# Performance work log

Measured on AMD Instinct MI355X. Metric: run time of the kernel, lower is better.

Reference implementation:

```python
import jax, jax.numpy as jnp
import numpy as np

B = 32       # batch
IN_N = 32    # input capsules
IN_D = 16    # input capsule dim (== out_d)
H = 14       # input spatial
OUT_N = 32   # output capsules
OUT_D = 16
HO = 7       # parent grid h_out = w_out
HID = 64     # Linformer projection dim
EPS = 1e-5


def _gconv(x, w, groups):
    # x: [b, C, H, W], w: [C_out, C_in/groups, kh, kw]; stride 1, pad 1
    return jax.lax.conv_general_dilated(
        x, w, window_strides=(1, 1), padding=((1, 1), (1, 1)),
        dimension_numbers=("NCHW", "OIHW", "NCHW"), feature_group_count=groups)


def setup_inputs() -> dict:
    key = jax.random.key(0)
    ks = jax.random.split(key, 7)
    current_pose = jax.random.normal(ks[0], (B, IN_N, H, H, IN_D), dtype=jnp.float32)
    next_pose = jax.random.normal(ks[1], (B, OUT_N, HO, HO, OUT_D), dtype=jnp.float32)
    # grouped conv weights (torch layout OIHW, groups = IN_N)
    current_w = 0.05 * jax.random.normal(ks[2], (IN_N * IN_D, IN_D, 3, 3), dtype=jnp.float32)
    next_w = 0.05 * jax.random.normal(ks[3], (OUT_N * OUT_D, OUT_N * OUT_D // IN_N, 3, 3), dtype=jnp.float32)
    E_proj = 0.02 * jax.random.normal(ks[4], (IN_N, H * H, HID), dtype=jnp.float32)
    rel_embedd = jax.random.normal(ks[5], (IN_D, HO * HO), dtype=jnp.float32)
    ln_gamma = jnp.ones((OUT_D,), dtype=jnp.float32)
    ln_beta = jnp.zeros((OUT_D,), dtype=jnp.float32)
    return {
        "current_pose": current_pose, "next_pose": next_pose,
        "current_w": current_w, "next_w": next_w,
        "E_proj": E_proj, "rel_embedd": rel_embedd,
        "ln_gamma": ln_gamma, "ln_beta": ln_beta,
        "num_iter": 1,
    }


def reference(current_pose, next_pose, current_w, next_w, E_proj, rel_embedd,
              ln_gamma, ln_beta, num_iter):
    b = current_pose.shape[0]
    # 5D -> [b, n*d, H, W]
    cp = current_pose.transpose(0, 2, 3, 1, 4).reshape(b, H, H, IN_N * IN_D)
    cp = cp.transpose(0, 3, 1, 2)
    cp = _gconv(cp, current_w, IN_N)                       # [b, n*d, H, H]
    # headwise Linformer key projection
    cp = cp.reshape(b, IN_D, IN_N, 1, H * H)
    k = jnp.matmul(cp, E_proj)                             # [b, d, n, 1, HID]
    k = k.reshape(b, IN_D, IN_N * HID).transpose(0, 2, 1)  # [b, n*HID, d]
    rel = jnp.broadcast_to(rel_embedd.T[None], (b, HO * HO, IN_D))
    k = jnp.concatenate([k, rel], axis=1)                  # [b, N, d]

    # parent pose -> queries
    q = next_pose.transpose(0, 2, 3, 1, 4).reshape(b, HO, HO, OUT_N * OUT_D)
    q = q.transpose(0, 3, 1, 2)
    q = _gconv(q, next_w, IN_N)                            # [b, out_n*out_d, HO, HO]
    q = q.reshape(b, OUT_N * HO * HO, OUT_D)               # [b, J, d]

    dots = jnp.einsum("bje,bie->bji", q, k) * (IN_D ** -0.5)  # [b, J, N]
    dots = jax.nn.softmax(dots, axis=-2)                   # softmax over queries j
    out = jnp.einsum("bji,bie->bje", dots, k)              # [b, J, d]

    out = out.reshape(b, OUT_N * IN_D, HO, HO)
    out = _gconv(out, next_w, IN_N)
    out = out.reshape(b, OUT_N, HO, HO, IN_D)

    # LayerNorm over last dim (dropout rate = 0)
    mu = out.mean(-1, keepdims=True)
    var = ((out - mu) ** 2).mean(-1, keepdims=True)
    out = (out - mu) / jnp.sqrt(var + EPS) * ln_gamma + ln_beta
    return out
```

## Files before the change

### kernel.cpp

```cpp
#include <hip/hip_runtime.h>

typedef unsigned short u16;
typedef __attribute__((ext_vector_type(8))) short short8;
typedef __attribute__((ext_vector_type(4))) float floatx4;

#define MFMA16(a, b, c) __builtin_amdgcn_mfma_f32_16x16x32_bf16(a, b, c, 0, 0, 0)

__device__ inline u16 bf16rn(float x) {
    unsigned u = __float_as_uint(x);
    u += 0x7fffu + ((u >> 16) & 1u);
    return (u16)(u >> 16);
}
__device__ inline float bf16tof(u16 h) { return __uint_as_float(((unsigned)h) << 16); }
__device__ inline short8 ld8(const u16* p) { return *(const short8*)p; }

__global__ __launch_bounds__(256) void k_ecvt2(const float* __restrict__ E,
                                               const float* __restrict__ rel,
                                               const float* __restrict__ w,
                                               u16* __restrict__ EhT,
                                               u16* __restrict__ ElT,
                                               u16* __restrict__ Kh,
                                               u16* __restrict__ Kl,
                                               u16* __restrict__ KhT,
                                               u16* __restrict__ KlT,
                                               float* __restrict__ w2) {
    int blk = blockIdx.x, tid = threadIdx.x;
    if (blk < 32) {
        __shared__ float ep[196 * 65];
        int m = blk;
        const float* eb = E + (size_t)m * 12544;
        for (int t = tid; t < 12544; t += 256) {
            int p = t >> 6, h = t & 63;
            ep[p * 65 + h] = eb[t];
        }
        __syncthreads();
        for (int t = tid; t < 64 * 224; t += 256) {
            int h = t / 224, p = t % 224;
            float v = (p < 196) ? ep[p * 65 + h] : 0.f;
            u16 hi = bf16rn(v);
            u16 lo = bf16rn(v - bf16tof(hi));
            EhT[(size_t)m * 14336 + t] = hi;
            ElT[(size_t)m * 14336 + t] = lo;
        }
    } else if (blk < 64) {
        int b = blk - 32;
        size_t bK = (size_t)b * 2112;
        size_t bT = (size_t)b * 33792;
#pragma unroll
        for (int k = 0; k < 4; ++k) {
            int idx = tid + k * 256;
            int row = idx >> 4, e = idx & 15;
            int i = 2048 + row;
            float v = (row < 49) ? rel[e * 49 + row] : 0.f;
            u16 h = bf16rn(v);
            u16 l = bf16rn(v - bf16tof(h));
            Kh[(bK + i) * 16 + e] = h;
            Kl[(bK + i) * 16 + e] = l;
            KhT[bT + (size_t)e * 2112 + i] = h;
            KlT[bT + (size_t)e * 2112 + i] = l;
        }
    } else {
        int g0 = (blk - 64) * 4;
        for (int t = tid; t < 4 * 2304; t += 256) {
            int g = g0 + t / 2304, r = t % 2304;
            int oc = r / 144, rr = r % 144;
            w2[(size_t)g * 2304 + (rr / 9) * 144 + oc * 9 + (rr % 9)] =
                w[(size_t)g * 2304 + r];
        }
    }
}

__global__ __launch_bounds__(256) void k_conv14(const float* __restrict__ pose,
                                                const float* __restrict__ w2,
                                                float* __restrict__ out) {
    int blk = blockIdx.x;
    int oh = blk & 1, bg = blk >> 1;
    int tid = threadIdx.x;
    __shared__ float patch[16 * 256];
#pragma unroll
    for (int k = 0; k < 16; ++k) patch[k * 256 + tid] = 0.f;
    __syncthreads();
    const float* pin = pose + (size_t)bg * 3136;
    for (int t = tid; t < 3136; t += 256) {
        int p = t >> 4, ic = t & 15;
        int y = p / 14, x = p % 14;
        patch[ic * 256 + (y + 1) * 16 + (x + 1)] = pin[t];
    }
    __syncthreads();
    int g = bg & 31;
    const float* wg = w2 + (size_t)g * 2304 + oh * 72;
    float* po = out + (size_t)bg * 3136 + oh * 8 * 196;
    if (tid < 196) {
        int y = tid / 14, x = tid % 14;
        int base = (y + 1) * 16 + (x + 1);
        float acc[8];
#pragma unroll
        for (int oc = 0; oc < 8; ++oc) acc[oc] = 0.f;
        for (int ic = 0; ic < 16; ++ic) {
            const float* pr = patch + ic * 256 + base;
            float win[9];
#pragma unroll
            for (int ky = 0; ky < 3; ++ky)
#pragma unroll
                for (int kx = 0; kx < 3; ++kx)
                    win[ky * 3 + kx] = pr[(ky - 1) * 16 + (kx - 1)];
            const float* wi = wg + ic * 144;
#pragma unroll
            for (int oc = 0; oc < 8; ++oc)
#pragma unroll
                for (int kk = 0; kk < 9; ++kk)
                    acc[oc] += win[kk] * wi[oc * 9 + kk];
        }
#pragma unroll
        for (int oc = 0; oc < 8; ++oc) po[oc * 196 + tid] = acc[oc];
    }
}

__global__ __launch_bounds__(64) void k_conv7(const float* __restrict__ in,
                                              const float* __restrict__ in2,
                                              const float* __restrict__ w,
                                              float* __restrict__ out, int mode) {
    int blk = blockIdx.x;
    int oh = blk & 1, bg = blk >> 1;
    int tid = threadIdx.x;
    __shared__ float patch[16 * 144];
    for (int t = tid; t < 16 * 144; t += 64) patch[t] = 0.f;
    __syncthreads();
    const float* pin = in + (size_t)bg * 784;
    if (mode == 1) {
        for (int t = tid; t < 784; t += 64) {
            int p = t >> 4, ic = t & 15;
            int y = p / 7, x = p % 7;
            patch[ic * 144 + (y + 1) * 16 + (x + 1)] = pin[t];
        }
    } else {
        const float* pin2 = in2 + (size_t)bg * 784;
        for (int t = tid; t < 784; t += 64) {
            int ic = t / 49, p = t % 49;
            int y = p / 7, x = p % 7;
            patch[ic * 144 + (y + 1) * 16 + (x + 1)] = pin[t] + pin2[t];
        }
    }
    __syncthreads();
    int g = bg & 31;
    const float* wg = w + (size_t)g * 2304 + (size_t)oh * 8 * 144;
    float* po = out + (size_t)bg * 784 + (size_t)oh * 8 * 49;
    if (tid < 49) {
        int y = tid / 7, x = tid % 7;
        int base = (y + 1) * 16 + (x + 1);
        float acc[8];
#pragma unroll
        for (int oc = 0; oc < 8; ++oc) acc[oc] = 0.f;
        for (int ic = 0; ic < 16; ++ic) {
            const float* pr = patch + ic * 144 + base;
            float win[9];
#pragma unroll
            for (int ky = 0; ky < 3; ++ky)
#pragma unroll
                for (int kx = 0; kx < 3; ++kx)
                    win[ky * 3 + kx] = pr[(ky - 1) * 16 + (kx - 1)];
            const float* wi = wg + ic * 9;
#pragma unroll
            for (int oc = 0; oc < 8; ++oc)
#pragma unroll
                for (int kk = 0; kk < 9; ++kk)
                    acc[oc] += win[kk] * wi[oc * 144 + kk];
        }
#pragma unroll
        for (int oc = 0; oc < 8; ++oc) po[oc * 49 + tid] = acc[oc];
    }
}

__global__ __launch_bounds__(256) void k_kproj2(const float* __restrict__ cpconv,
                                                const u16* __restrict__ EhT,
                                                const u16* __restrict__ ElT,
                                                u16* __restrict__ Kh,
                                                u16* __restrict__ Kl,
                                                u16* __restrict__ KhT,
                                                u16* __restrict__ KlT) {
    int blk = blockIdx.x;
    int b = blk >> 5, m = blk & 31;
    int wave = threadIdx.x >> 6, lane = threadIdx.x & 63;
    int ht = wave;
    int n = lane & 15, quad = lane >> 4;

    const float* arow = cpconv + ((size_t)b * 512 + (size_t)n * 32 + m) * 196;
    const u16* bhrow = EhT + ((size_t)m * 64 + ht * 16 + n) * 224;
    const u16* blrow = ElT + ((size_t)m * 64 + ht * 16 + n) * 224;

    floatx4 c = {0.f, 0.f, 0.f, 0.f};
#pragma unroll
    for (int pc = 0; pc < 7; ++pc) {
        int p0 = pc * 32 + quad * 8;
        float av[8];
        if (p0 <= 188) {
            float4 x = *(const float4*)(arow + p0);
            float4 y = *(const float4*)(arow + p0 + 4);
            av[0]=x.x; av[1]=x.y; av[2]=x.z; av[3]=x.w;
            av[4]=y.x; av[5]=y.y; av[6]=y.z; av[7]=y.w;
        } else {
#pragma unroll
            for (int k2 = 0; k2 < 8; ++k2) av[k2] = (p0 + k2 < 196) ? arow[p0 + k2] : 0.f;
        }
        short8 ah, al;
#pragma unroll
        for (int k2 = 0; k2 < 8; ++k2) {
            u16 h = bf16rn(av[k2]);
            ah[k2] = (short)h;
            al[k2] = (short)bf16rn(av[k2] - bf16tof(h));
        }
        short8 bh = ld8(bhrow + pc * 32 + quad * 8);
        short8 bl = ld8(blrow + pc * 32 + quad * 8);
        c = MFMA16(ah, bh, c);
        c = MFMA16(ah, bl, c);
        c = MFMA16(al, bh, c);
    }
    int i = m * 64 + ht * 16 + n;
    size_t bK = (size_t)b * 2112;
    size_t bT = (size_t)b * 33792;
    u16 h[4], l[4];
#pragma unroll
    for (int r = 0; r < 4; ++r) {
        h[r] = bf16rn(c[r]);
        l[r] = bf16rn(c[r] - bf16tof(h[r]));
    }
    *(uint2*)(Kh + (bK + i) * 16 + quad * 4) =
        make_uint2((unsigned)h[0] | ((unsigned)h[1] << 16), (unsigned)h[2] | ((unsigned)h[3] << 16));
    *(uint2*)(Kl + (bK + i) * 16 + quad * 4) =
        make_uint2((unsigned)l[0] | ((unsigned)l[1] << 16), (unsigned)l[2] | ((unsigned)l[3] << 16));
#pragma unroll
    for (int r = 0; r < 4; ++r) {
        KhT[bT + (size_t)(quad * 4 + r) * 2112 + i] = h[r];
        KlT[bT + (size_t)(quad * 4 + r) * 2112 + i] = l[r];
    }
}

__global__ __launch_bounds__(256) void k_cvt(const float* __restrict__ qconv,
                                             u16* __restrict__ Qp) {
    int gid = blockIdx.x * 256 + threadIdx.x;
    const float4* q4 = (const float4*)(qconv + (size_t)gid * 16);
    float4 t0 = q4[0], t1 = q4[1], t2 = q4[2], t3 = q4[3];
    float v[16] = {t0.x,t0.y,t0.z,t0.w, t1.x,t1.y,t1.z,t1.w,
                   t2.x,t2.y,t2.z,t2.w, t3.x,t3.y,t3.z,t3.w};
    unsigned hw[8], lw[8];
#pragma unroll
    for (int t = 0; t < 8; ++t) {
        float x0 = v[2*t] * 0.25f, x1 = v[2*t+1] * 0.25f;
        u16 h0 = bf16rn(x0), h1 = bf16rn(x1);
        u16 l0 = bf16rn(x0 - bf16tof(h0)), l1 = bf16rn(x1 - bf16tof(h1));
        hw[t] = (unsigned)h0 | ((unsigned)h1 << 16);
        lw[t] = (unsigned)l0 | ((unsigned)l1 << 16);
    }
    uint4* r4 = (uint4*)(Qp + (size_t)gid * 32);
    r4[0] = make_uint4(hw[0], hw[1], hw[2], hw[3]);
    r4[1] = make_uint4(hw[4], hw[5], hw[6], hw[7]);
    r4[2] = make_uint4(lw[0], lw[1], lw[2], lw[3]);
    r4[3] = make_uint4(lw[4], lw[5], lw[6], lw[7]);
}

__global__ __launch_bounds__(256) void k_stats4(const u16* __restrict__ Qp,
                                                const u16* __restrict__ Kh,
                                                const u16* __restrict__ Kl,
                                                float* __restrict__ dpart) {
    int blk = blockIdx.x;
    int b = blk / 34; int rem = blk % 34; int jh = rem / 17; int tb = rem % 17;
    int wave = threadIdx.x >> 6, lane = threadIdx.x & 63;
    int it2 = tb * 4 + wave;
    if (it2 >= 66) return;
    int ibase = it2 * 32;
    int n = lane & 15, quad = lane >> 4;
    size_t bK = (size_t)b * 2112;
    const u16* kb = Kh + (bK + ibase + n) * 16 + (quad & 1) * 8;
    const u16* lb = Kl + (bK + ibase + n) * 16 + (quad & 1) * 8;
    short8 bh0 = ld8(kb), bh1 = ld8(kb + 256);
    short8 bl0 = ld8(lb), bl1 = ld8(lb + 256);
    const u16* qb = Qp + (size_t)b * 50176 + (size_t)jh * 49 * 512 + n * 32 + quad * 8;
    floatx4 d0 = {0.f,0.f,0.f,0.f}, d1 = {0.f,0.f,0.f,0.f};
    short8 a0 = ld8(qb), a1 = ld8(qb + 512);
    for (int c = 0; c < 49; ++c) {
        short8 a2 = (c + 2 < 49) ? ld8(qb + (size_t)(c + 2) * 512) : a0;
        floatx4 s0 = {0.f,0.f,0.f,0.f}, s1 = {0.f,0.f,0.f,0.f};
        s0 = MFMA16(a0, bh0, s0);
        s0 = MFMA16(a0, bl0, s0);
        s1 = MFMA16(a0, bh1, s1);
        s1 = MFMA16(a0, bl1, s1);
        d0.x += __expf(s0.x); d0.y += __expf(s0.y);
        d0.z += __expf(s0.z); d0.w += __expf(s0.w);
        d1.x += __expf(s1.x); d1.y += __expf(s1.y);
        d1.z += __expf(s1.z); d1.w += __expf(s1.w);
        a0 = a1; a1 = a2;
    }
    float t0 = d0.x + d0.y + d0.z + d0.w;
    float t1 = d1.x + d1.y + d1.z + d1.w;
    t0 += __shfl_xor(t0, 16); t0 += __shfl_xor(t0, 32);
    t1 += __shfl_xor(t1, 16); t1 += __shfl_xor(t1, 32);
    if (quad == 0) {
        dpart[(size_t)jh * 67584 + bK + ibase + n]      = t0;
        dpart[(size_t)jh * 67584 + bK + ibase + 16 + n] = t1;
    }
}

__global__ __launch_bounds__(256) void k_pv5(const u16* __restrict__ Qp,
                                             const u16* __restrict__ Kh,
                                             const u16* __restrict__ Kl,
                                             const u16* __restrict__ KhT,
                                             const u16* __restrict__ KlT,
                                             const float* __restrict__ dpart,
                                             float* __restrict__ opart) {
    __shared__ __align__(16) u16 sH[2][32][16];
    __shared__ __align__(16) u16 sL[2][32][16];
    __shared__ __align__(16) u16 tH[2][16][32];
    __shared__ __align__(16) u16 tL[2][16][32];
    __shared__ __align__(16) u16 w16[4][16][40];
    __shared__ float rll[2][32];

    int blk = blockIdx.x;
    int b = blk / 50; int rem = blk % 50; int jtb = rem >> 1; int ih = rem & 1;
    int tid = threadIdx.x, wave = tid >> 6, lane = tid & 63;
    int n = lane & 15, quad = lane >> 4, qh = quad & 1;
    int jt = jtb * 4 + wave;
    int jtc = jt < 98 ? jt : 97;
    int i0 = ih * 1056;
    size_t bK = (size_t)b * 2112;
    size_t bT = (size_t)b * 33792;
    const float* d0p = dpart + bK;
    const float* d1p = dpart + 67584 + bK;

    short8 aq = ld8(Qp + ((size_t)b * 1568 + (size_t)jtc * 16 + n) * 32 + quad * 8);

    int role = wave, L = lane;
    uint4 sreg; float dv = 1.f;
    auto ldchunk = [&](int c) {
        int i0c = i0 + c * 32;
        if (role == 0)      sreg = *(const uint4*)(Kh  + (bK + i0c + (L >> 1)) * 16 + (L & 1) * 8);
        else if (role == 1) sreg = *(const uint4*)(Kl  + (bK + i0c + (L >> 1)) * 16 + (L & 1) * 8);
        else if (role == 2) sreg = *(const uint4*)(KhT + bT + (size_t)(L >> 2) * 2112 + i0c + (L & 3) * 8);
        else {
            sreg = *(const uint4*)(KlT + bT + (size_t)(L >> 2) * 2112 + i0c + (L & 3) * 8);
            if (L < 32) dv = d0p[i0c + L] + d1p[i0c + L];
        }
    };
    auto stchunk = [&](int bf) {
        if (role == 0)      *(uint4*)(&sH[bf][L >> 1][(L & 1) * 8]) = sreg;
        else if (role == 1) *(uint4*)(&sL[bf][L >> 1][(L & 1) * 8]) = sreg;
        else if (role == 2) *(uint4*)(&tH[bf][L >> 2][(L & 3) * 8]) = sreg;
        else {
            *(uint4*)(&tL[bf][L >> 2][(L & 3) * 8]) = sreg;
            if (L < 32) rll[bf][L] = 1.0f / dv;
        }
    };

    floatx4 o = {0.f, 0.f, 0.f, 0.f};

    ldchunk(0); stchunk(0); ldchunk(1);
    __syncthreads();
    for (int c = 0; c < 33; ++c) {
        int cb = c & 1;
        short8 sh0 = ld8(&sH[cb][n][qh * 8]);
        short8 sh1 = ld8(&sH[cb][16 + n][qh * 8]);
        short8 sl0 = ld8(&sL[cb][n][qh * 8]);
        short8 sl1 = ld8(&sL[cb][16 + n][qh * 8]);
        short8 th  = ld8(&tH[cb][n][quad * 8]);
        short8 tl  = ld8(&tL[cb][n][quad * 8]);
        float r0 = rll[cb][n], r1 = rll[cb][16 + n];
        floatx4 s0 = {0.f,0.f,0.f,0.f};
        s0 = MFMA16(aq, sh0, s0);
        s0 = MFMA16(aq, sl0, s0);
        floatx4 s1 = {0.f,0.f,0.f,0.f};
        s1 = MFMA16(aq, sh1, s1);
        s1 = MFMA16(aq, sl1, s1);
#pragma unroll
        for (int r = 0; r < 4; ++r) {
            float w0 = __expf(s0[r]) * r0;
            float w1 = __expf(s1[r]) * r1;
            w16[wave][quad * 4 + r][n]      = (u16)(__float_as_uint(w0) >> 16);
            w16[wave][quad * 4 + r][16 + n] = (u16)(__float_as_uint(w1) >> 16);
        }
        asm volatile("s_waitcnt lgkmcnt(0)" ::: "memory");
        short8 aw = ld8(&w16[wave][n][quad * 8]);
        o = MFMA16(aw, th, o);
        o = MFMA16(aw, tl, o);
        if (c < 32) stchunk((c + 1) & 1);
        if (c < 31) ldchunk(c + 2);
        __syncthreads();
    }
    if (jt < 98) {
        float* ob = opart + (size_t)ih * 802816 + ((size_t)b * 1568 + (size_t)jt * 16) * 16;
#pragma unroll
        for (int r = 0; r < 4; ++r) ob[(quad * 4 + r) * 16 + n] = o[r];
    }
}

__global__ __launch_bounds__(256) void k_ln(const float* __restrict__ x,
                                            const float* __restrict__ gamma,
                                            const float* __restrict__ beta,
                                            float* __restrict__ out, int ngroups) {
    int g = blockIdx.x * 256 + threadIdx.x;
    if (g >= ngroups) return;
    const float4* xp = (const float4*)(x + (size_t)g * 16);
    float4 x0 = xp[0], x1 = xp[1], x2 = xp[2], x3 = xp[3];
    float sum = x0.x + x0.y + x0.z + x0.w + x1.x + x1.y + x1.z + x1.w
              + x2.x + x2.y + x2.z + x2.w + x3.x + x3.y + x3.z + x3.w;
    float mu = sum * 0.0625f;
    float var = 0.f;
    var += (x0.x-mu)*(x0.x-mu) + (x0.y-mu)*(x0.y-mu) + (x0.z-mu)*(x0.z-mu) + (x0.w-mu)*(x0.w-mu);
    var += (x1.x-mu)*(x1.x-mu) + (x1.y-mu)*(x1.y-mu) + (x1.z-mu)*(x1.z-mu) + (x1.w-mu)*(x1.w-mu);
    var += (x2.x-mu)*(x2.x-mu) + (x2.y-mu)*(x2.y-mu) + (x2.z-mu)*(x2.z-mu) + (x2.w-mu)*(x2.w-mu);
    var += (x3.x-mu)*(x3.x-mu) + (x3.y-mu)*(x3.y-mu) + (x3.z-mu)*(x3.z-mu) + (x3.w-mu)*(x3.w-mu);
    float rstd = rsqrtf(var * 0.0625f + 1e-5f);
    const float4* gp = (const float4*)gamma;
    const float4* bp = (const float4*)beta;
    float4 g0 = gp[0], g1 = gp[1], g2 = gp[2], g3 = gp[3];
    float4 be0 = bp[0], be1 = bp[1], be2 = bp[2], be3 = bp[3];
    float4 o0, o1, o2, o3;
    o0.x = (x0.x-mu)*rstd*g0.x + be0.x; o0.y = (x0.y-mu)*rstd*g0.y + be0.y;
    o0.z = (x0.z-mu)*rstd*g0.z + be0.z; o0.w = (x0.w-mu)*rstd*g0.w + be0.w;
    o1.x = (x1.x-mu)*rstd*g1.x + be1.x; o1.y = (x1.y-mu)*rstd*g1.y + be1.y;
    o1.z = (x1.z-mu)*rstd*g1.z + be1.z; o1.w = (x1.w-mu)*rstd*g1.w + be1.w;
    o2.x = (x2.x-mu)*rstd*g2.x + be2.x; o2.y = (x2.y-mu)*rstd*g2.y + be2.y;
    o2.z = (x2.z-mu)*rstd*g2.z + be2.z; o2.w = (x2.w-mu)*rstd*g2.w + be2.w;
    o3.x = (x3.x-mu)*rstd*g3.x + be3.x; o3.y = (x3.y-mu)*rstd*g3.y + be3.y;
    o3.z = (x3.z-mu)*rstd*g3.z + be3.z; o3.w = (x3.w-mu)*rstd*g3.w + be3.w;
    float4* op = (float4*)(out + (size_t)g * 16);
    op[0] = o0; op[1] = o1; op[2] = o2; op[3] = o3;
}

extern "C" void kernel_launch(void* const* d_in, const int* in_sizes, int n_in,
                              void* d_out, int out_size, void* d_ws, size_t ws_size,
                              hipStream_t stream) {
    const float* current_pose = (const float*)d_in[0];
    const float* next_pose    = (const float*)d_in[1];
    const float* current_w    = (const float*)d_in[2];
    const float* next_w       = (const float*)d_in[3];
    const float* E_proj       = (const float*)d_in[4];
    const float* rel          = (const float*)d_in[5];
    const float* ln_gamma     = (const float*)d_in[6];
    const float* ln_beta      = (const float*)d_in[7];
    float* out = (float*)d_out;
    float* ws  = (float*)d_ws;

    float* cpconv = ws;
    float* conv2  = ws;
    float* opart  = ws + 802816;
    float* dpart  = ws + 2408448;
    float* qconv  = ws + 3211264;
    float* w2     = ws + 4014080;
    u16*   ub     = (u16*)(ws + 4087808);
    u16* Qp  = ub;
    u16* Kh  = ub + 1605632;
    u16* Kl  = ub + 2686976;
    u16* KhT = ub + 3768320;
    u16* KlT = ub + 4849664;
    u16* EhT = ub + 5931008;
    u16* ElT = ub + 6389760;

    k_ecvt2 <<<72,   256, 0, stream>>>(E_proj, rel, current_w, EhT, ElT,
                                       Kh, Kl, KhT, KlT, w2);
    k_conv14<<<2048, 256, 0, stream>>>(current_pose, w2, cpconv);
    k_conv7 <<<2048, 64,  0, stream>>>(next_pose, next_pose, next_w, qconv, 1);
    k_cvt   <<<196,  256, 0, stream>>>(qconv, Qp);
    k_kproj2<<<1024, 256, 0, stream>>>(cpconv, EhT, ElT, Kh, Kl, KhT, KlT);
    k_stats4<<<1088, 256, 0, stream>>>(Qp, Kh, Kl, dpart);
    k_pv5   <<<1600, 256, 0, stream>>>(Qp, Kh, Kl, KhT, KlT, dpart, opart);
    k_conv7 <<<2048, 64,  0, stream>>>(opart, opart + 802816, next_w, conv2, 0);
    k_ln    <<<196,  256, 0, stream>>>(conv2, ln_gamma, ln_beta, out, 50176);
}
```

Baseline: 232.3 us.

## Fuse q-conv with bf16 split, conv with layernorm, prescale K, pipeline PV loop

The query conv now writes split-bf16 Q directly, which removes the separate conversion kernel and its fp32 round trip. The output conv is fused with LayerNorm and sums three partial buffers. A new k_kscale kernel folds the per-key softmax denominators into the transposed K once, so the PV loop no longer divides by them. The PV kernel splits the key range three ways instead of two and software-pipelines the second MFMA pair one chunk behind. The cost is an extra kernel launch plus a K rewrite pass, more blocks, and K rounding applied twice.

```diff
diff --git a/kernel.cpp b/kernel.cpp
--- a/kernel.cpp
+++ b/kernel.cpp
@@ -116,37 +116,27 @@
     }
 }
 
-__global__ __launch_bounds__(64) void k_conv7(const float* __restrict__ in,
-                                              const float* __restrict__ in2,
-                                              const float* __restrict__ w,
-                                              float* __restrict__ out, int mode) {
-    int blk = blockIdx.x;
-    int oh = blk & 1, bg = blk >> 1;
+__global__ __launch_bounds__(128) void k_conv7q(const float* __restrict__ pose,
+                                                const float* __restrict__ w,
+                                                u16* __restrict__ Qp) {
+    int bg = blockIdx.x;
     int tid = threadIdx.x;
     __shared__ float patch[16 * 144];
-    for (int t = tid; t < 16 * 144; t += 64) patch[t] = 0.f;
-    __syncthreads();
-    const float* pin = in + (size_t)bg * 784;
-    if (mode == 1) {
-        for (int t = tid; t < 784; t += 64) {
-            int p = t >> 4, ic = t & 15;
-            int y = p / 7, x = p % 7;
-            patch[ic * 144 + (y + 1) * 16 + (x + 1)] = pin[t];
-        }
-    } else {
-        const float* pin2 = in2 + (size_t)bg * 784;
-        for (int t = tid; t < 784; t += 64) {
-            int ic = t / 49, p = t % 49;
-            int y = p / 7, x = p % 7;
-            patch[ic * 144 + (y + 1) * 16 + (x + 1)] = pin[t] + pin2[t];
-        }
+    __shared__ float cvout[784];
+    for (int t = tid; t < 16 * 144; t += 128) patch[t] = 0.f;
+    __syncthreads();
+    const float* pin = pose + (size_t)bg * 784;
+    for (int t = tid; t < 784; t += 128) {
+        int p = t >> 4, ic = t & 15;
+        int y = p / 7, x = p % 7;
+        patch[ic * 144 + (y + 1) * 16 + (x + 1)] = pin[t];
     }
     __syncthreads();
     int g = bg & 31;
+    int oh = tid >> 6, lt = tid & 63;
     const float* wg = w + (size_t)g * 2304 + (size_t)oh * 8 * 144;
-    float* po = out + (size_t)bg * 784 + (size_t)oh * 8 * 49;
-    if (tid < 49) {
-        int y = tid / 7, x = tid % 7;
+    if (lt < 49) {
+        int y = lt / 7, x = lt % 7;
         int base = (y + 1) * 16 + (x + 1);
         float acc[8];
 #pragma unroll
@@ -167,7 +157,28 @@
                     acc[oc] += win[kk] * wi[oc * 144 + kk];
         }
 #pragma unroll
-        for (int oc = 0; oc < 8; ++oc) po[oc * 49 + tid] = acc[oc];
+        for (int oc = 0; oc < 8; ++oc) cvout[(oh * 8 + oc) * 49 + lt] = acc[oc];
+    }
+    __syncthreads();
+    if (tid < 49) {
+        float v[16];
+#pragma unroll
+        for (int k = 0; k < 16; ++k) v[k] = cvout[tid * 16 + k];
+        unsigned hw[8], lw[8];
+#pragma unroll
+        for (int t = 0; t < 8; ++t) {
+            float x0 = v[2*t] * 0.25f, x1 = v[2*t+1] * 0.25f;
+            u16 h0 = bf16rn(x0), h1 = bf16rn(x1);
+            u16 l0 = bf16rn(x0 - bf16tof(h0)), l1 = bf16rn(x1 - bf16tof(h1));
+            hw[t] = (unsigned)h0 | ((unsigned)h1 << 16);
+            lw[t] = (unsigned)l0 | ((unsigned)l1 << 16);
+        }
+        size_t j = (size_t)bg * 49 + tid;
+        uint4* r4 = (uint4*)(Qp + j * 32);
+        r4[0] = make_uint4(hw[0], hw[1], hw[2], hw[3]);
+        r4[1] = make_uint4(hw[4], hw[5], hw[6], hw[7]);
+        r4[2] = make_uint4(lw[0], lw[1], lw[2], lw[3]);
+        r4[3] = make_uint4(lw[4], lw[5], lw[6], lw[7]);
     }
 }
 
@@ -233,29 +244,6 @@
         KhT[bT + (size_t)(quad * 4 + r) * 2112 + i] = h[r];
         KlT[bT + (size_t)(quad * 4 + r) * 2112 + i] = l[r];
     }
-}
-
-__global__ __launch_bounds__(256) void k_cvt(const float* __restrict__ qconv,
-                                             u16* __restrict__ Qp) {
-    int gid = blockIdx.x * 256 + threadIdx.x;
-    const float4* q4 = (const float4*)(qconv + (size_t)gid * 16);
-    float4 t0 = q4[0], t1 = q4[1], t2 = q4[2], t3 = q4[3];
-    float v[16] = {t0.x,t0.y,t0.z,t0.w, t1.x,t1.y,t1.z,t1.w,
-                   t2.x,t2.y,t2.z,t2.w, t3.x,t3.y,t3.z,t3.w};
-    unsigned hw[8], lw[8];
-#pragma unroll
-    for (int t = 0; t < 8; ++t) {
-        float x0 = v[2*t] * 0.25f, x1 = v[2*t+1] * 0.25f;
-        u16 h0 = bf16rn(x0), h1 = bf16rn(x1);
-        u16 l0 = bf16rn(x0 - bf16tof(h0)), l1 = bf16rn(x1 - bf16tof(h1));
-        hw[t] = (unsigned)h0 | ((unsigned)h1 << 16);
-        lw[t] = (unsigned)l0 | ((unsigned)l1 << 16);
-    }
-    uint4* r4 = (uint4*)(Qp + (size_t)gid * 32);
-    r4[0] = make_uint4(hw[0], hw[1], hw[2], hw[3]);
-    r4[1] = make_uint4(hw[4], hw[5], hw[6], hw[7]);
-    r4[2] = make_uint4(lw[0], lw[1], lw[2], lw[3]);
-    r4[3] = make_uint4(lw[4], lw[5], lw[6], lw[7]);
 }
 
 __global__ __launch_bounds__(256) void k_stats4(const u16* __restrict__ Qp,
@@ -300,89 +288,125 @@
     }
 }
 
-__global__ __launch_bounds__(256) void k_pv5(const u16* __restrict__ Qp,
+__global__ __launch_bounds__(256) void k_kscale(const float* __restrict__ dpart,
+                                                u16* __restrict__ KhT,
+                                                u16* __restrict__ KlT) {
+    int blk = blockIdx.x;
+    int b = blk >> 2, q = blk & 3;
+    int tid = threadIdx.x;
+    size_t bT = (size_t)b * 33792;
+    const float* d0 = dpart + (size_t)b * 2112;
+    const float* d1 = dpart + 67584 + (size_t)b * 2112;
+    for (int t = tid; t < 1056; t += 256) {
+        int v = q * 1056 + t;
+        int e = v / 264, i8 = (v % 264) * 8;
+        size_t off = bT + (size_t)e * 2112 + i8;
+        uint4 hv = *(uint4*)(KhT + off);
+        uint4 lv = *(uint4*)(KlT + off);
+        float4 da = *(const float4*)(d0 + i8), db = *(const float4*)(d0 + i8 + 4);
+        float4 ea = *(const float4*)(d1 + i8), eb = *(const float4*)(d1 + i8 + 4);
+        float rl[8] = {1.f/(da.x+ea.x), 1.f/(da.y+ea.y), 1.f/(da.z+ea.z), 1.f/(da.w+ea.w),
+                       1.f/(db.x+eb.x), 1.f/(db.y+eb.y), 1.f/(db.z+eb.z), 1.f/(db.w+eb.w)};
+        unsigned hu[4] = {hv.x, hv.y, hv.z, hv.w};
+        unsigned lu[4] = {lv.x, lv.y, lv.z, lv.w};
+        unsigned ho[4], lo4[4];
+#pragma unroll
+        for (int k = 0; k < 4; ++k) {
+            u16 h0 = (u16)hu[k], h1 = (u16)(hu[k] >> 16);
+            u16 l0 = (u16)lu[k], l1 = (u16)(lu[k] >> 16);
+            float v0 = (bf16tof(h0) + bf16tof(l0)) * rl[2*k];
+            float v1 = (bf16tof(h1) + bf16tof(l1)) * rl[2*k+1];
+            u16 nh0 = bf16rn(v0), nh1 = bf16rn(v1);
+            u16 nl0 = bf16rn(v0 - bf16tof(nh0)), nl1 = bf16rn(v1 - bf16tof(nh1));
+            ho[k]  = (unsigned)nh0 | ((unsigned)nh1 << 16);
+            lo4[k] = (unsigned)nl0 | ((unsigned)nl1 << 16);
+        }
+        *(uint4*)(KhT + off) = make_uint4(ho[0], ho[1], ho[2], ho[3]);
+        *(uint4*)(KlT + off) = make_uint4(lo4[0], lo4[1], lo4[2], lo4[3]);
+    }
+}
+
+__global__ __launch_bounds__(256) void k_pv6(const u16* __restrict__ Qp,
                                              const u16* __restrict__ Kh,
                                              const u16* __restrict__ Kl,
                                              const u16* __restrict__ KhT,
                                              const u16* __restrict__ KlT,
-                                             const float* __restrict__ dpart,
                                              float* __restrict__ opart) {
     __shared__ __align__(16) u16 sH[2][32][16];
     __shared__ __align__(16) u16 sL[2][32][16];
     __shared__ __align__(16) u16 tH[2][16][32];
     __shared__ __align__(16) u16 tL[2][16][32];
-    __shared__ __align__(16) u16 w16[4][16][40];
-    __shared__ float rll[2][32];
+    __shared__ __align__(16) u16 w16[4][2][16][40];
 
     int blk = blockIdx.x;
-    int b = blk / 50; int rem = blk % 50; int jtb = rem >> 1; int ih = rem & 1;
+    int b = blk / 75; int rem = blk % 75; int jtb = rem / 3; int ih = rem % 3;
     int tid = threadIdx.x, wave = tid >> 6, lane = tid & 63;
     int n = lane & 15, quad = lane >> 4, qh = quad & 1;
     int jt = jtb * 4 + wave;
     int jtc = jt < 98 ? jt : 97;
-    int i0 = ih * 1056;
+    int i0 = ih * 704;
     size_t bK = (size_t)b * 2112;
     size_t bT = (size_t)b * 33792;
-    const float* d0p = dpart + bK;
-    const float* d1p = dpart + 67584 + bK;
 
     short8 aq = ld8(Qp + ((size_t)b * 1568 + (size_t)jtc * 16 + n) * 32 + quad * 8);
 
     int role = wave, L = lane;
-    uint4 sreg; float dv = 1.f;
+    uint4 sreg;
     auto ldchunk = [&](int c) {
         int i0c = i0 + c * 32;
         if (role == 0)      sreg = *(const uint4*)(Kh  + (bK + i0c + (L >> 1)) * 16 + (L & 1) * 8);
         else if (role == 1) sreg = *(const uint4*)(Kl  + (bK + i0c + (L >> 1)) * 16 + (L & 1) * 8);
         else if (role == 2) sreg = *(const uint4*)(KhT + bT + (size_t)(L >> 2) * 2112 + i0c + (L & 3) * 8);
-        else {
-            sreg = *(const uint4*)(KlT + bT + (size_t)(L >> 2) * 2112 + i0c + (L & 3) * 8);
-            if (L < 32) dv = d0p[i0c + L] + d1p[i0c + L];
-        }
+        else                sreg = *(const uint4*)(KlT + bT + (size_t)(L >> 2) * 2112 + i0c + (L & 3) * 8);
     };
     auto stchunk = [&](int bf) {
         if (role == 0)      *(uint4*)(&sH[bf][L >> 1][(L & 1) * 8]) = sreg;
         else if (role == 1) *(uint4*)(&sL[bf][L >> 1][(L & 1) * 8]) = sreg;
         else if (role == 2) *(uint4*)(&tH[bf][L >> 2][(L & 3) * 8]) = sreg;
-        else {
-            *(uint4*)(&tL[bf][L >> 2][(L & 3) * 8]) = sreg;
-            if (L < 32) rll[bf][L] = 1.0f / dv;
-        }
+        else                *(uint4*)(&tL[bf][L >> 2][(L & 3) * 8]) = sreg;
     };
 
     floatx4 o = {0.f, 0.f, 0.f, 0.f};
+    short8 thp = {}, tlp = {};
 
     ldchunk(0); stchunk(0); ldchunk(1);
     __syncthreads();
-    for (int c = 0; c < 33; ++c) {
+    for (int c = 0; c < 22; ++c) {
         int cb = c & 1;
+        short8 th  = ld8(&tH[cb][n][quad * 8]);
+        short8 tl  = ld8(&tL[cb][n][quad * 8]);
         short8 sh0 = ld8(&sH[cb][n][qh * 8]);
         short8 sh1 = ld8(&sH[cb][16 + n][qh * 8]);
         short8 sl0 = ld8(&sL[cb][n][qh * 8]);
         short8 sl1 = ld8(&sL[cb][16 + n][qh * 8]);
-        short8 th  = ld8(&tH[cb][n][quad * 8]);
-        short8 tl  = ld8(&tL[cb][n][quad * 8]);
-        float r0 = rll[cb][n], r1 = rll[cb][16 + n];
+        short8 aw = {};
+        if (c > 0) aw = ld8(&w16[wave][1 - cb][n][quad * 8]);
         floatx4 s0 = {0.f,0.f,0.f,0.f};
         s0 = MFMA16(aq, sh0, s0);
         s0 = MFMA16(aq, sl0, s0);
         floatx4 s1 = {0.f,0.f,0.f,0.f};
         s1 = MFMA16(aq, sh1, s1);
         s1 = MFMA16(aq, sl1, s1);
+        if (c > 0) {
+            o = MFMA16(aw, thp, o);
+            o = MFMA16(aw, tlp, o);
+        }
 #pragma unroll
         for (int r = 0; r < 4; ++r) {
-            float w0 = __expf(s0[r]) * r0;
-            float w1 = __expf(s1[r]) * r1;
-            w16[wave][quad * 4 + r][n]      = (u16)(__float_as_uint(w0) >> 16);
-            w16[wave][quad * 4 + r][16 + n] = (u16)(__float_as_uint(w1) >> 16);
-        }
-        asm volatile("s_waitcnt lgkmcnt(0)" ::: "memory");
-        short8 aw = ld8(&w16[wave][n][quad * 8]);
-        o = MFMA16(aw, th, o);
-        o = MFMA16(aw, tl, o);
-        if (c < 32) stchunk((c + 1) & 1);
-        if (c < 31) ldchunk(c + 2);
+            float w0 = __expf(s0[r]);
+            float w1 = __expf(s1[r]);
+            w16[wave][cb][quad * 4 + r][n]      = (u16)(__float_as_uint(w0) >> 16);
+            w16[wave][cb][quad * 4 + r][16 + n] = (u16)(__float_as_uint(w1) >> 16);
+        }
+        thp = th; tlp = tl;
+        if (c + 1 < 22) stchunk((c + 1) & 1);
+        if (c + 2 < 22) ldchunk(c + 2);
         __syncthreads();
+    }
+    {
+        short8 aw = ld8(&w16[wave][1][n][quad * 8]);
+        o = MFMA16(aw, thp, o);
+        o = MFMA16(aw, tlp, o);
     }
     if (jt < 98) {
         float* ob = opart + (size_t)ih * 802816 + ((size_t)b * 1568 + (size_t)jt * 16) * 16;
@@ -391,38 +415,73 @@
     }
 }
 
-__global__ __launch_bounds__(256) void k_ln(const float* __restrict__ x,
-                                            const float* __restrict__ gamma,
-                                            const float* __restrict__ beta,
-                                            float* __restrict__ out, int ngroups) {
-    int g = blockIdx.x * 256 + threadIdx.x;
-    if (g >= ngroups) return;
-    const float4* xp = (const float4*)(x + (size_t)g * 16);
-    float4 x0 = xp[0], x1 = xp[1], x2 = xp[2], x3 = xp[3];
-    float sum = x0.x + x0.y + x0.z + x0.w + x1.x + x1.y + x1.z + x1.w
-              + x2.x + x2.y + x2.z + x2.w + x3.x + x3.y + x3.z + x3.w;
-    float mu = sum * 0.0625f;
-    float var = 0.f;
-    var += (x0.x-mu)*(x0.x-mu) + (x0.y-mu)*(x0.y-mu) + (x0.z-mu)*(x0.z-mu) + (x0.w-mu)*(x0.w-mu);
-    var += (x1.x-mu)*(x1.x-mu) + (x1.y-mu)*(x1.y-mu) + (x1.z-mu)*(x1.z-mu) + (x1.w-mu)*(x1.w-mu);
-    var += (x2.x-mu)*(x2.x-mu) + (x2.y-mu)*(x2.y-mu) + (x2.z-mu)*(x2.z-mu) + (x2.w-mu)*(x2.w-mu);
-    var += (x3.x-mu)*(x3.x-mu) + (x3.y-mu)*(x3.y-mu) + (x3.z-mu)*(x3.z-mu) + (x3.w-mu)*(x3.w-mu);
-    float rstd = rsqrtf(var * 0.0625f + 1e-5f);
-    const float4* gp = (const float4*)gamma;
-    const float4* bp = (const float4*)beta;
-    float4 g0 = gp[0], g1 = gp[1], g2 = gp[2], g3 = gp[3];
-    float4 be0 = bp[0], be1 = bp[1], be2 = bp[2], be3 = bp[3];
-    float4 o0, o1, o2, o3;
-    o0.x = (x0.x-mu)*rstd*g0.x + be0.x; o0.y = (x0.y-mu)*rstd*g0.y + be0.y;
-    o0.z = (x0.z-mu)*rstd*g0.z + be0.z; o0.w = (x0.w-mu)*rstd*g0.w + be0.w;
-    o1.x = (x1.x-mu)*rstd*g1.x + be1.x; o1.y = (x1.y-mu)*rstd*g1.y + be1.y;
-    o1.z = (x1.z-mu)*rstd*g1.z + be1.z; o1.w = (x1.w-mu)*rstd*g1.w + be1.w;
-    o2.x = (x2.x-mu)*rstd*g2.x + be2.x; o2.y = (x2.y-mu)*rstd*g2.y + be2.y;
-    o2.z = (x2.z-mu)*rstd*g2.z + be2.z; o2.w = (x2.w-mu)*rstd*g2.w + be2.w;
-    o3.x = (x3.x-mu)*rstd*g3.x + be3.x; o3.y = (x3.y-mu)*rstd*g3.y + be3.y;
-    o3.z = (x3.z-mu)*rstd*g3.z + be3.z; o3.w = (x3.w-mu)*rstd*g3.w + be3.w;
-    float4* op = (float4*)(out + (size_t)g * 16);
-    op[0] = o0; op[1] = o1; op[2] = o2; op[3] = o3;
+__global__ __launch_bounds__(128) void k_conv7ln(const float* __restrict__ op0,
+                                                 const float* __restrict__ op1,
+                                                 const float* __restrict__ op2,
+                                                 const float* __restrict__ w,
+                                                 const float* __restrict__ gamma,
+                                                 const float* __restrict__ beta,
+                                                 float* __restrict__ out) {
+    int bg = blockIdx.x;
+    int tid = threadIdx.x;
+    __shared__ float patch[16 * 144];
+    __shared__ float cvout[784];
+    for (int t = tid; t < 16 * 144; t += 128) patch[t] = 0.f;
+    __syncthreads();
+    const float* p0 = op0 + (size_t)bg * 784;
+    const float* p1 = op1 + (size_t)bg * 784;
+    const float* p2 = op2 + (size_t)bg * 784;
+    for (int t = tid; t < 784; t += 128) {
+        int ic = t / 49, p = t % 49;
+        int y = p / 7, x = p % 7;
+        patch[ic * 144 + (y + 1) * 16 + (x + 1)] = p0[t] + p1[t] + p2[t];
+    }
+    __syncthreads();
+    int g = bg & 31;
+    int oh = tid >> 6, lt = tid & 63;
+    const float* wg = w + (size_t)g * 2304 + (size_t)oh * 8 * 144;
+    if (lt < 49) {
+        int y = lt / 7, x = lt % 7;
+        int base = (y + 1) * 16 + (x + 1);
+        float acc[8];
+#pragma unroll
+        for (int oc = 0; oc < 8; ++oc) acc[oc] = 0.f;
+        for (int ic = 0; ic < 16; ++ic) {
+            const float* pr = patch + ic * 144 + base;
+            float win[9];
+#pragma unroll
+            for (int ky = 0; ky < 3; ++ky)
+#pragma unroll
+                for (int kx = 0; kx < 3; ++kx)
+                    win[ky * 3 + kx] = pr[(ky - 1) * 16 + (kx - 1)];
+            const float* wi = wg + ic * 9;
+#pragma unroll
+            for (int oc = 0; oc < 8; ++oc)
+#pragma unroll
+                for (int kk = 0; kk < 9; ++kk)
+                    acc[oc] += win[kk] * wi[oc * 144 + kk];
+        }
+#pragma unroll
+        for (int oc = 0; oc < 8; ++oc) cvout[(oh * 8 + oc) * 49 + lt] = acc[oc];
+    }
+    __syncthreads();
+    if (tid < 49) {
+        float v[16];
+        float sum = 0.f;
+#pragma unroll
+        for (int k = 0; k < 16; ++k) { v[k] = cvout[tid * 16 + k]; sum += v[k]; }
+        float mu = sum * 0.0625f;
+        float var = 0.f;
+#pragma unroll
+        for (int k = 0; k < 16; ++k) { float d = v[k] - mu; var += d * d; }
+        float rstd = rsqrtf(var * 0.0625f + 1e-5f);
+        float4 o4[4];
+#pragma unroll
+        for (int k = 0; k < 16; ++k)
+            ((float*)o4)[k] = (v[k] - mu) * rstd * gamma[k] + beta[k];
+        float4* po = (float4*)(out + (size_t)bg * 784 + (size_t)tid * 16);
+        po[0] = o4[0]; po[1] = o4[1]; po[2] = o4[2]; po[3] = o4[3];
+    }
 }
 
 extern "C" void kernel_launch(void* const* d_in, const int* in_sizes, int n_in,
@@ -440,12 +499,10 @@
     float* ws  = (float*)d_ws;
 
     float* cpconv = ws;
-    float* conv2  = ws;
-    float* opart  = ws + 802816;
+    float* opart  = ws;
     float* dpart  = ws + 2408448;
-    float* qconv  = ws + 3211264;
-    float* w2     = ws + 4014080;
-    u16*   ub     = (u16*)(ws + 4087808);
+    float* w2     = ws + 3211264;
+    u16*   ub     = (u16*)(ws + 3284992);
     u16* Qp  = ub;
     u16* Kh  = ub + 1605632;
     u16* Kl  = ub + 2686976;
@@ -454,14 +511,15 @@
     u16* EhT = ub + 5931008;
     u16* ElT = ub + 6389760;
 
-    k_ecvt2 <<<72,   256, 0, stream>>>(E_proj, rel, current_w, EhT, ElT,
-                                       Kh, Kl, KhT, KlT, w2);
-    k_conv14<<<2048, 256, 0, stream>>>(current_pose, w2, cpconv);
-    k_conv7 <<<2048, 64,  0, stream>>>(next_pose, next_pose, next_w, qconv, 1);
-    k_cvt   <<<196,  256, 0, stream>>>(qconv, Qp);
-    k_kproj2<<<1024, 256, 0, stream>>>(cpconv, EhT, ElT, Kh, Kl, KhT, KlT);
-    k_stats4<<<1088, 256, 0, stream>>>(Qp, Kh, Kl, dpart);
-    k_pv5   <<<1600, 256, 0, stream>>>(Qp, Kh, Kl, KhT, KlT, dpart, opart);
-    k_conv7 <<<2048, 64,  0, stream>>>(opart, opart + 802816, next_w, conv2, 0);
-    k_ln    <<<196,  256, 0, stream>>>(conv2, ln_gamma, ln_beta, out, 50176);
-}
+    k_ecvt2  <<<72,   256, 0, stream>>>(E_proj, rel, current_w, EhT, ElT,
+                                        Kh, Kl, KhT, KlT, w2);
+    k_conv14 <<<2048, 256, 0, stream>>>(current_pose, w2, cpconv);
+    k_conv7q <<<1024, 128, 0, stream>>>(next_pose, next_w, Qp);
+    k_kproj2 <<<1024, 256, 0, stream>>>(cpconv, EhT, ElT, Kh, Kl, KhT, KlT);
+    k_stats4 <<<1088, 256, 0, stream>>>(Qp, Kh, Kl, dpart);
+    k_kscale <<<128,  256, 0, stream>>>(dpart, KhT, KlT);
+    k_pv6    <<<2400, 256, 0, stream>>>(Qp, Kh, Kl, KhT, KlT, opart);
+    k_conv7ln<<<1024, 128, 0, stream>>>(opart, opart + 802816, opart + 1605632,
+                                        next_w, ln_gamma, ln_beta, out);
+    (void)in_sizes; (void)n_in; (void)out_size; (void)ws_size;
+}
```

After: 235.9 us. Within noise of the previous version (+1.5%).
